# Kernel tuning notes

Measured on AMD Instinct MI355X. Metric: run time of the kernel, lower is better.

The kernel has to match this reference:

```python
import jax, jax.numpy as jnp
import numpy as np

NUM_DOMAINS = 8
MARGIN = 1.0


def setup_inputs() -> dict:
    key = jax.random.key(0)
    k1, k2 = jax.random.split(key)
    features = jax.random.normal(k1, (4096, 1024), dtype=jnp.float32)
    domain_labels = jax.random.randint(k2, (4096,), 0, NUM_DOMAINS)
    return {"features": features, "domain_labels": domain_labels}


def reference(features, domain_labels):
    # Full BxB euclidean distance matrix (matches torch.cdist p=2, which uses
    # the mm-based path for this size). Safe sqrt so diagonal zeros are exact.
    sq = jnp.sum(features * features, axis=-1)                      # (B,)
    d2 = sq[:, None] + sq[None, :] - 2.0 * (features @ features.T)  # (B,B)
    d2 = jnp.maximum(d2, 0.0)
    dist = jnp.where(d2 > 0, jnp.sqrt(jnp.where(d2 > 0, d2, 1.0)), 0.0)
    vals = jax.nn.relu(MARGIN - dist)                               # (B,B)

    # Per-domain pair sums via one-hot contraction: s_d = m_d^T V m_d.
    onehot = (domain_labels[:, None] == jnp.arange(NUM_DOMAINS)[None, :]
              ).astype(features.dtype)                              # (B,K)
    n = onehot.sum(axis=0)                                          # (K,)
    row_sums = vals @ onehot                                        # (B,K)
    pair_sums = (onehot * row_sums).sum(axis=0)                     # (K,)

    valid = n > 1  # torch loop skips singleton domains
    per_domain = jnp.where(valid, pair_sums / jnp.maximum(n * n, 1.0), 0.0)
    cnt = valid.sum().astype(features.dtype)
    return jnp.where(cnt > 0, per_domain.sum() / jnp.maximum(cnt, 1.0), 0.0)
```

## Files before the change

### kernel.cpp

```cpp
#include <hip/hip_runtime.h>

#define NDOM 8
#define TT   64
#define KDIM 1024
#define RPAD 1040
#define BMAX 4096
#define GGRID 512

typedef float f32x4 __attribute__((ext_vector_type(4)));

__device__ inline void gload16(const void* g, void* l) {
    __builtin_amdgcn_global_load_lds(
        (const __attribute__((address_space(1))) unsigned int*)g,
        (__attribute__((address_space(3))) unsigned int*)l, 16, 0, 0);
}

__global__ __launch_bounds__(256) void k_prep(
    const float* __restrict__ F, const int* __restrict__ labels, int B,
    unsigned char* __restrict__ Fb, float* __restrict__ sq,
    int* __restrict__ perm, int* __restrict__ dom_off) {
    const int t = threadIdx.x, lane = t & 63, wv = t >> 6;

    if (blockIdx.x == 0) {
        __shared__ int lab[BMAX];
        __shared__ unsigned wcnt[4][NDOM];
        for (int i = t; i < BMAX; i += 256) lab[i] = (i < B) ? labels[i] : -1;
        __syncthreads();

        int nch = (B + 63) >> 6;
        int cpw = (nch + 3) >> 2;
        int c0 = wv * cpw, c1 = min(c0 + cpw, nch);
        unsigned long long below = (1ull << lane) - 1ull;

        unsigned cnt[NDOM];
#pragma unroll
        for (int d = 0; d < NDOM; ++d) cnt[d] = 0;
        for (int c = c0; c < c1; ++c) {
            int d = lab[c * 64 + lane];
#pragma unroll
            for (int dd = 0; dd < NDOM; ++dd)
                cnt[dd] += (unsigned)__popcll(__ballot(d == dd));
        }
        if (lane == 0)
#pragma unroll
            for (int dd = 0; dd < NDOM; ++dd) wcnt[wv][dd] = cnt[dd];
        __syncthreads();

        unsigned offs[NDOM + 1];
        offs[0] = 0;
#pragma unroll
        for (int dd = 0; dd < NDOM; ++dd)
            offs[dd + 1] = offs[dd] + wcnt[0][dd] + wcnt[1][dd] + wcnt[2][dd] + wcnt[3][dd];
        if (t <= NDOM) dom_off[t] = (int)offs[t];

        unsigned run[NDOM];
#pragma unroll
        for (int dd = 0; dd < NDOM; ++dd) {
            unsigned base = offs[dd];
            for (int w = 0; w < 4; ++w)
                if (w < wv) base += wcnt[w][dd];
            run[dd] = base;
        }
        for (int c = c0; c < c1; ++c) {
            int i = c * 64 + lane;
            int d = lab[i];
            int pos = -1;
#pragma unroll
            for (int dd = 0; dd < NDOM; ++dd) {
                unsigned long long m = __ballot(d == dd);
                if (d == dd) pos = (int)run[dd] + __popcll(m & below);
                run[dd] += (unsigned)__popcll(m);
            }
            if (i < B) perm[pos] = i;
        }
        return;
    }

    int i0 = (int)(blockIdx.x - 1) * 16;
    for (int j = wv; j < 16; j += 4) {
        int row = i0 + j;
        if (row >= B) break;
        const float4* srow = (const float4*)(F + (size_t)row * KDIM);
        int* drow = (int*)(Fb + (size_t)row * KDIM);
        float ss = 0.f;
#pragma unroll
        for (int it = 0; it < 4; ++it) {
            float4 v = srow[it * 64 + lane];
            ss += v.x * v.x + v.y * v.y + v.z * v.z + v.w * v.w;
            int p = __builtin_amdgcn_cvt_pk_fp8_f32(v.x, v.y, 0, false);
            p = __builtin_amdgcn_cvt_pk_fp8_f32(v.z, v.w, p, true);
            drow[it * 64 + lane] = p;
        }
#pragma unroll
        for (int s = 32; s > 0; s >>= 1) ss += __shfl_xor(ss, s);
        if (lane == 0) sq[row] = ss;
    }
}

__global__ __launch_bounds__(256) void k_gram(
    const unsigned char* __restrict__ Fb, const float* __restrict__ sq,
    const int* __restrict__ perm, const int* __restrict__ dom_off,
    float* __restrict__ part) {
    __shared__ __align__(16) unsigned char lA[TT * RPAD];
    __shared__ __align__(16) unsigned char lB[TT * RPAD];
    __shared__ int s_p[128];
    __shared__ float s_sq[128];
    __shared__ int s_offs[NDOM + 1], s_ts[NDOM + 1];
    __shared__ float s_ps[NDOM];

    const int t = threadIdx.x, lane = t & 63, wv = t >> 6;
    const int m16 = lane & 15, quad = lane >> 4;
    const int wm = (wv & 1) * 32, wn = (wv >> 1) * 32;

    if (t == 0) {
        int T = 0;
        for (int d = 0; d < NDOM; ++d) {
            int o0 = dom_off[d], o1 = dom_off[d + 1];
            s_offs[d] = o0;
            s_ts[d] = T;
            int n = o1 - o0;
            int nt = (n + TT - 1) / TT;
            T += nt * (nt + 1) / 2;
        }
        s_offs[NDOM] = dom_off[NDOM];
        s_ts[NDOM] = T;
    }
    if (t < NDOM) s_ps[t] = 0.f;
    __syncthreads();
    const int T = s_ts[NDOM];

    for (int tile = blockIdx.x; tile < T; tile += gridDim.x) {
        int dom = 0;
        while (tile >= s_ts[dom + 1]) ++dom;
        int off = s_offs[dom], n = s_offs[dom + 1] - off;
        int nt = (n + TT - 1) / TT;
        int rel = tile - s_ts[dom];
        int ty = 0, rem = rel;
        while (rem >= nt - ty) { rem -= nt - ty; ++ty; }
        int tx = ty + rem;
        int tr = ty * TT, tc = tx * TT;
        bool diag = (ty == tx);

        if (t < 128) {
            int r = (t < 64) ? min(tr + t, n - 1) : min(tc + (t - 64), n - 1);
            int p = perm[off + r];
            s_p[t] = p;
            s_sq[t] = sq[p];
        }
        __syncthreads();

#pragma unroll
        for (int j = 0; j < 16; ++j) {
            int r = wv * 16 + j;
            gload16(Fb + (size_t)s_p[r] * KDIM + lane * 16, lA + r * RPAD);
            if (!diag)
                gload16(Fb + (size_t)s_p[64 + r] * KDIM + lane * 16, lB + r * RPAD);
        }
        __syncthreads();

        const unsigned char* Bb = diag ? lA : lB;
        const unsigned char* pa0 = lA + (wm + m16) * RPAD + quad * 8;
        const unsigned char* pa1 = lA + (wm + 16 + m16) * RPAD + quad * 8;
        const unsigned char* pb0 = Bb + (wn + m16) * RPAD + quad * 8;
        const unsigned char* pb1 = Bb + (wn + 16 + m16) * RPAD + quad * 8;
        f32x4 a00 = (f32x4){0.f, 0.f, 0.f, 0.f};
        f32x4 a01 = (f32x4){0.f, 0.f, 0.f, 0.f};
        f32x4 a10 = (f32x4){0.f, 0.f, 0.f, 0.f};
        f32x4 a11 = (f32x4){0.f, 0.f, 0.f, 0.f};
#pragma unroll
        for (int ks = 0; ks < 32; ++ks) {
            long av0 = *(const long*)(pa0 + ks * 32);
            long av1 = *(const long*)(pa1 + ks * 32);
            long bv0 = *(const long*)(pb0 + ks * 32);
            long bv1 = *(const long*)(pb1 + ks * 32);
            a00 = __builtin_amdgcn_mfma_f32_16x16x32_fp8_fp8(av0, bv0, a00, 0, 0, 0);
            a01 = __builtin_amdgcn_mfma_f32_16x16x32_fp8_fp8(av0, bv1, a01, 0, 0, 0);
            a10 = __builtin_amdgcn_mfma_f32_16x16x32_fp8_fp8(av1, bv0, a10, 0, 0, 0);
            a11 = __builtin_amdgcn_mfma_f32_16x16x32_fp8_fp8(av1, bv1, a11, 0, 0, 0);
        }

        float local = 0.f;
#pragma unroll
        for (int im = 0; im < 2; ++im) {
            int lr0 = wm + im * 16 + quad * 4;
#pragma unroll
            for (int in = 0; in < 2; ++in) {
                f32x4 av = (im == 0) ? ((in == 0) ? a00 : a01)
                                     : ((in == 0) ? a10 : a11);
                int lc = wn + in * 16 + m16;
                int pc = tc + lc;
                if (pc >= n) continue;
                float sb = s_sq[64 + lc];
#pragma unroll
                for (int r = 0; r < 4; ++r) {
                    int pr = tr + lr0 + r;
                    if (pr < n) {
                        float val;
                        if (pr == pc) {
                            val = 1.0f;
                        } else {
                            float d2 = s_sq[lr0 + r] + sb - 2.0f * av[r];
                            d2 = fmaxf(d2, 0.f);
                            val = fmaxf(1.0f - sqrtf(d2), 0.f);
                        }
                        local += val;
                    }
                }
            }
        }
        if (!diag) local *= 2.f;
#pragma unroll
        for (int s = 32; s > 0; s >>= 1) local += __shfl_xor(local, s);
        if (lane == 0) atomicAdd(&s_ps[dom], local);
        __syncthreads();
    }

    __syncthreads();
    if (t < NDOM) part[blockIdx.x * NDOM + t] = s_ps[t];
}

__global__ __launch_bounds__(256) void k_final(
    const float* __restrict__ part, const int* __restrict__ dom_off,
    float* __restrict__ out) {
    __shared__ float red[8][32];
    int t = threadIdx.x;
    int d = t & 7, ch = t >> 3;
    float s = 0.f;
    for (int b = ch; b < GGRID; b += 32) s += part[b * NDOM + d];
    red[d][ch] = s;
    __syncthreads();
    if (t == 0) {
        float acc = 0.f;
        int v = 0;
        for (int dd = 0; dd < NDOM; ++dd) {
            int n = dom_off[dd + 1] - dom_off[dd];
            if (n > 1) {
                float ps = 0.f;
                for (int c = 0; c < 32; ++c) ps += red[dd][c];
                acc += ps / ((float)n * (float)n);
                ++v;
            }
        }
        out[0] = (v > 0) ? acc / (float)v : 0.f;
    }
}

extern "C" void kernel_launch(void* const* d_in, const int* in_sizes, int n_in,
                              void* d_out, int out_size, void* d_ws, size_t ws_size,
                              hipStream_t stream) {
    const float* F = (const float*)d_in[0];
    const int* labels = (const int*)d_in[1];
    int B = in_sizes[1];

    char* ws = (char*)d_ws;
    unsigned char* Fb = (unsigned char*)ws;
    float* sq = (float*)(ws + (size_t)BMAX * KDIM);
    int* perm = (int*)(ws + (size_t)BMAX * KDIM + BMAX * 4);
    int* dom_off = (int*)(ws + (size_t)BMAX * KDIM + BMAX * 8);
    float* part = (float*)(ws + (size_t)BMAX * KDIM + BMAX * 8 + 256);

    int ncv = (B + 15) / 16;
    k_prep<<<ncv + 1, 256, 0, stream>>>(F, labels, B, Fb, sq, perm, dom_off);
    k_gram<<<GGRID, 256, 0, stream>>>(Fb, sq, perm, dom_off, part);
    k_final<<<1, 256, 0, stream>>>(part, dom_off, (float*)d_out);
}
```

Measured before the change: 97.78 us.

## Split gram tiles along K into two halves and fuse final reduction

Each 64x64 tile's K=1024 reduction is split into two K-halves computed by separate blocks, which doubles the work items and halves shared-memory use per block. The partial accumulators are written to a global scratch buffer, and a second kernel sums them and applies the distance/margin epilogue. The separate final kernel is replaced by a last-block-done atomic counter inside phase 2. This trades a round trip of partial results through global memory and an extra launch for more parallelism and occupancy.

Result: slower. 105.0 us (+7.4%).

```diff
diff --git a/kernel.cpp b/kernel.cpp
--- a/kernel.cpp
+++ b/kernel.cpp
@@ -3,7 +3,8 @@
 #define NDOM 8
 #define TT   64
 #define KDIM 1024
-#define RPAD 1040
+#define KH   512
+#define PSTR 1040
 #define BMAX 4096
 #define GGRID 512
 
@@ -15,10 +16,40 @@
         (__attribute__((address_space(3))) unsigned int*)l, 16, 0, 0);
 }
 
+__device__ inline void build_tables(const int* dom_off, int* s_offs, int* s_ts) {
+    int T = 0;
+    for (int d = 0; d < NDOM; ++d) {
+        int o0 = dom_off[d], o1 = dom_off[d + 1];
+        s_offs[d] = o0;
+        s_ts[d] = T;
+        int n = o1 - o0;
+        int nt = (n + TT - 1) / TT;
+        T += nt * (nt + 1) / 2;
+    }
+    s_offs[NDOM] = dom_off[NDOM];
+    s_ts[NDOM] = T;
+}
+
+__device__ inline void decode_tile(const int* s_offs, const int* s_ts, int tile,
+                                   int& off, int& n, int& tr, int& tc,
+                                   int& dom, bool& diag) {
+    dom = 0;
+    while (tile >= s_ts[dom + 1]) ++dom;
+    off = s_offs[dom];
+    n = s_offs[dom + 1] - off;
+    int nt = (n + TT - 1) / TT;
+    int rel = tile - s_ts[dom];
+    int ty = 0, rem = rel;
+    while (rem >= nt - ty) { rem -= nt - ty; ++ty; }
+    int tx = ty + rem;
+    tr = ty * TT; tc = tx * TT;
+    diag = (ty == tx);
+}
+
 __global__ __launch_bounds__(256) void k_prep(
     const float* __restrict__ F, const int* __restrict__ labels, int B,
     unsigned char* __restrict__ Fb, float* __restrict__ sq,
-    int* __restrict__ perm, int* __restrict__ dom_off) {
+    int* __restrict__ perm, int* __restrict__ dom_off, unsigned* __restrict__ bar) {
     const int t = threadIdx.x, lane = t & 63, wv = t >> 6;
 
     if (blockIdx.x == 0) {
@@ -52,6 +83,7 @@
         for (int dd = 0; dd < NDOM; ++dd)
             offs[dd + 1] = offs[dd] + wcnt[0][dd] + wcnt[1][dd] + wcnt[2][dd] + wcnt[3][dd];
         if (t <= NDOM) dom_off[t] = (int)offs[t];
+        if (t == 0) { bar[0] = 0u; bar[1] = 0u; }
 
         unsigned run[NDOM];
 #pragma unroll
@@ -97,78 +129,62 @@
     }
 }
 
-__global__ __launch_bounds__(256) void k_gram(
-    const unsigned char* __restrict__ Fb, const float* __restrict__ sq,
-    const int* __restrict__ perm, const int* __restrict__ dom_off,
-    float* __restrict__ part) {
-    __shared__ __align__(16) unsigned char lA[TT * RPAD];
-    __shared__ __align__(16) unsigned char lB[TT * RPAD];
+__global__ __launch_bounds__(256) void k_phase1(
+    const unsigned char* __restrict__ Fb, const int* __restrict__ perm,
+    const int* __restrict__ dom_off, float* __restrict__ pacc) {
+    __shared__ __align__(16) unsigned char lA[32 * PSTR];
+    __shared__ __align__(16) unsigned char lB[32 * PSTR];
     __shared__ int s_p[128];
-    __shared__ float s_sq[128];
     __shared__ int s_offs[NDOM + 1], s_ts[NDOM + 1];
-    __shared__ float s_ps[NDOM];
 
     const int t = threadIdx.x, lane = t & 63, wv = t >> 6;
     const int m16 = lane & 15, quad = lane >> 4;
     const int wm = (wv & 1) * 32, wn = (wv >> 1) * 32;
 
-    if (t == 0) {
-        int T = 0;
-        for (int d = 0; d < NDOM; ++d) {
-            int o0 = dom_off[d], o1 = dom_off[d + 1];
-            s_offs[d] = o0;
-            s_ts[d] = T;
-            int n = o1 - o0;
-            int nt = (n + TT - 1) / TT;
-            T += nt * (nt + 1) / 2;
-        }
-        s_offs[NDOM] = dom_off[NDOM];
-        s_ts[NDOM] = T;
-    }
-    if (t < NDOM) s_ps[t] = 0.f;
+    if (t == 0) build_tables(dom_off, s_offs, s_ts);
     __syncthreads();
     const int T = s_ts[NDOM];
 
-    for (int tile = blockIdx.x; tile < T; tile += gridDim.x) {
-        int dom = 0;
-        while (tile >= s_ts[dom + 1]) ++dom;
-        int off = s_offs[dom], n = s_offs[dom + 1] - off;
-        int nt = (n + TT - 1) / TT;
-        int rel = tile - s_ts[dom];
-        int ty = 0, rem = rel;
-        while (rem >= nt - ty) { rem -= nt - ty; ++ty; }
-        int tx = ty + rem;
-        int tr = ty * TT, tc = tx * TT;
-        bool diag = (ty == tx);
+    for (int half = blockIdx.x; half < 2 * T; half += gridDim.x) {
+        int tile = half >> 1, h = half & 1;
+        int off, n, tr, tc, dom;
+        bool diag;
+        decode_tile(s_offs, s_ts, tile, off, n, tr, tc, dom, diag);
 
         if (t < 128) {
             int r = (t < 64) ? min(tr + t, n - 1) : min(tc + (t - 64), n - 1);
-            int p = perm[off + r];
-            s_p[t] = p;
-            s_sq[t] = sq[p];
-        }
-        __syncthreads();
-
-#pragma unroll
-        for (int j = 0; j < 16; ++j) {
-            int r = wv * 16 + j;
-            gload16(Fb + (size_t)s_p[r] * KDIM + lane * 16, lA + r * RPAD);
-            if (!diag)
-                gload16(Fb + (size_t)s_p[64 + r] * KDIM + lane * 16, lB + r * RPAD);
+            s_p[t] = perm[off + r];
+        }
+        __syncthreads();
+
+#pragma unroll
+        for (int j = 0; j < 8; ++j) {
+            int pair = wv * 8 + j;
+            int rsel = pair * 2 + (lane >> 5);
+            const unsigned char* ga =
+                Fb + (size_t)s_p[rsel] * KDIM + h * KH + (lane & 31) * 16;
+            gload16(ga, lA + pair * PSTR);
+            if (!diag) {
+                const unsigned char* gb =
+                    Fb + (size_t)s_p[64 + rsel] * KDIM + h * KH + (lane & 31) * 16;
+                gload16(gb, lB + pair * PSTR);
+            }
         }
         __syncthreads();
 
         const unsigned char* Bb = diag ? lA : lB;
-        const unsigned char* pa0 = lA + (wm + m16) * RPAD + quad * 8;
-        const unsigned char* pa1 = lA + (wm + 16 + m16) * RPAD + quad * 8;
-        const unsigned char* pb0 = Bb + (wn + m16) * RPAD + quad * 8;
-        const unsigned char* pb1 = Bb + (wn + 16 + m16) * RPAD + quad * 8;
+        int rA0 = wm + m16, rA1 = wm + 16 + m16;
+        int rB0 = wn + m16, rB1 = wn + 16 + m16;
+        const unsigned char* pa0 = lA + (rA0 >> 1) * PSTR + (rA0 & 1) * KH + quad * 8;
+        const unsigned char* pa1 = lA + (rA1 >> 1) * PSTR + (rA1 & 1) * KH + quad * 8;
+        const unsigned char* pb0 = Bb + (rB0 >> 1) * PSTR + (rB0 & 1) * KH + quad * 8;
+        const unsigned char* pb1 = Bb + (rB1 >> 1) * PSTR + (rB1 & 1) * KH + quad * 8;
         f32x4 a00 = (f32x4){0.f, 0.f, 0.f, 0.f};
         f32x4 a01 = (f32x4){0.f, 0.f, 0.f, 0.f};
         f32x4 a10 = (f32x4){0.f, 0.f, 0.f, 0.f};
         f32x4 a11 = (f32x4){0.f, 0.f, 0.f, 0.f};
 #pragma unroll
-        for (int ks = 0; ks < 32; ++ks) {
+        for (int ks = 0; ks < 16; ++ks) {
             long av0 = *(const long*)(pa0 + ks * 32);
             long av1 = *(const long*)(pa1 + ks * 32);
             long bv0 = *(const long*)(pb0 + ks * 32);
@@ -178,6 +194,50 @@
             a10 = __builtin_amdgcn_mfma_f32_16x16x32_fp8_fp8(av1, bv0, a10, 0, 0, 0);
             a11 = __builtin_amdgcn_mfma_f32_16x16x32_fp8_fp8(av1, bv1, a11, 0, 0, 0);
         }
+
+        f32x4* dst = (f32x4*)pacc + (size_t)half * 1024 + wv * 256 + lane * 4;
+        dst[0] = a00; dst[1] = a01; dst[2] = a10; dst[3] = a11;
+        __syncthreads();
+    }
+}
+
+__global__ __launch_bounds__(256) void k_phase2(
+    const float* __restrict__ pacc, const float* __restrict__ sq,
+    const int* __restrict__ perm, const int* __restrict__ dom_off,
+    float* __restrict__ part, unsigned* __restrict__ bar,
+    float* __restrict__ out) {
+    __shared__ float s_sq[128];
+    __shared__ int s_offs[NDOM + 1], s_ts[NDOM + 1];
+    __shared__ float s_ps[NDOM];
+    __shared__ float red[NDOM][33];
+    __shared__ unsigned s_last;
+
+    const int t = threadIdx.x, lane = t & 63, wv = t >> 6;
+    const int m16 = lane & 15, quad = lane >> 4;
+    const int wm = (wv & 1) * 32, wn = (wv >> 1) * 32;
+
+    if (t == 0) build_tables(dom_off, s_offs, s_ts);
+    if (t < NDOM) s_ps[t] = 0.f;
+    __syncthreads();
+    const int T = s_ts[NDOM];
+
+    for (int tile = blockIdx.x; tile < T; tile += gridDim.x) {
+        int off, n, tr, tc, dom;
+        bool diag;
+        decode_tile(s_offs, s_ts, tile, off, n, tr, tc, dom, diag);
+
+        if (t < 128) {
+            int r = (t < 64) ? min(tr + t, n - 1) : min(tc + (t - 64), n - 1);
+            s_sq[t] = sq[perm[off + r]];
+        }
+        __syncthreads();
+
+        const f32x4* p0 = (const f32x4*)pacc + (size_t)(tile * 2) * 1024 + wv * 256 + lane * 4;
+        const f32x4* p1 = p0 + 1024;
+        f32x4 a00 = p0[0] + p1[0];
+        f32x4 a01 = p0[1] + p1[1];
+        f32x4 a10 = p0[2] + p1[2];
+        f32x4 a11 = p0[3] + p1[3];
 
         float local = 0.f;
 #pragma unroll
@@ -217,31 +277,37 @@
 
     __syncthreads();
     if (t < NDOM) part[blockIdx.x * NDOM + t] = s_ps[t];
-}
-
-__global__ __launch_bounds__(256) void k_final(
-    const float* __restrict__ part, const int* __restrict__ dom_off,
-    float* __restrict__ out) {
-    __shared__ float red[8][32];
-    int t = threadIdx.x;
-    int d = t & 7, ch = t >> 3;
-    float s = 0.f;
-    for (int b = ch; b < GGRID; b += 32) s += part[b * NDOM + d];
-    red[d][ch] = s;
     __syncthreads();
     if (t == 0) {
-        float acc = 0.f;
-        int v = 0;
-        for (int dd = 0; dd < NDOM; ++dd) {
-            int n = dom_off[dd + 1] - dom_off[dd];
-            if (n > 1) {
-                float ps = 0.f;
-                for (int c = 0; c < 32; ++c) ps += red[dd][c];
-                acc += ps / ((float)n * (float)n);
-                ++v;
+        __threadfence();
+        unsigned old = atomicAdd(&bar[1], 1u);
+        s_last = (old == (unsigned)gridDim.x - 1) ? 1u : 0u;
+    }
+    __syncthreads();
+    if (s_last) {
+        if (t == 0) __threadfence();
+        __syncthreads();
+        int d = t & 7, ch = t >> 3;
+        float s = 0.f;
+        for (int b = ch; b < GGRID; b += 32)
+            s += __hip_atomic_load(&part[b * NDOM + d], __ATOMIC_RELAXED,
+                                   __HIP_MEMORY_SCOPE_AGENT);
+        red[d][ch] = s;
+        __syncthreads();
+        if (t == 0) {
+            float acc = 0.f;
+            int v = 0;
+            for (int dd = 0; dd < NDOM; ++dd) {
+                int n = s_offs[dd + 1] - s_offs[dd];
+                if (n > 1) {
+                    float ps = 0.f;
+                    for (int c = 0; c < 32; ++c) ps += red[dd][c];
+                    acc += ps / ((float)n * (float)n);
+                    ++v;
+                }
             }
-        }
-        out[0] = (v > 0) ? acc / (float)v : 0.f;
+            out[0] = (v > 0) ? acc / (float)v : 0.f;
+        }
     }
 }
 
@@ -254,13 +320,15 @@
 
     char* ws = (char*)d_ws;
     unsigned char* Fb = (unsigned char*)ws;
-    float* sq = (float*)(ws + (size_t)BMAX * KDIM);
-    int* perm = (int*)(ws + (size_t)BMAX * KDIM + BMAX * 4);
-    int* dom_off = (int*)(ws + (size_t)BMAX * KDIM + BMAX * 8);
-    float* part = (float*)(ws + (size_t)BMAX * KDIM + BMAX * 8 + 256);
+    float* sq = (float*)(ws + 0x400000);
+    int* perm = (int*)(ws + 0x404000);
+    int* dom_off = (int*)(ws + 0x408000);
+    unsigned* bar = (unsigned*)(ws + 0x408100);
+    float* part = (float*)(ws + 0x409000);
+    float* pacc = (float*)(ws + 0x500000);
 
     int ncv = (B + 15) / 16;
-    k_prep<<<ncv + 1, 256, 0, stream>>>(F, labels, B, Fb, sq, perm, dom_off);
-    k_gram<<<GGRID, 256, 0, stream>>>(Fb, sq, perm, dom_off, part);
-    k_final<<<1, 256, 0, stream>>>(part, dom_off, (float*)d_out);
-}
+    k_prep<<<ncv + 1, 256, 0, stream>>>(F, labels, B, Fb, sq, perm, dom_off, bar);
+    k_phase1<<<GGRID, 256, 0, stream>>>(Fb, perm, dom_off, pacc);
+    k_phase2<<<GGRID, 256, 0, stream>>>(pacc, sq, perm, dom_off, part, bar, (float*)d_out);
+}
```
